# Optimization experiments

Hardware: AMD Instinct MI355X
Metric: run time of the kernel (lower is better)

Reference implementation:

```python
import jax, jax.numpy as jnp
import numpy as np

B, T, D_IN, N, O = 64, 512, 256, 1024, 128


def setup_inputs() -> dict:
    key = jax.random.key(0)
    k1, k2, k3, k4, k5 = jax.random.split(key, 5)
    X = jax.random.normal(k1, (B, T, D_IN), dtype=jnp.float32)
    # scale recurrent/input weights so tanh does not fully saturate
    Win = jax.random.normal(k2, (D_IN, N), dtype=jnp.float32) / np.sqrt(D_IN)
    W = jax.random.normal(k3, (N, N), dtype=jnp.float32) / np.sqrt(N)
    Wout = jax.random.normal(k4, (N, O), dtype=jnp.float32) / np.sqrt(N)
    bout = jax.random.normal(k5, (O,), dtype=jnp.float32)
    return {"X": X, "Win": Win, "W": W, "Wout": Wout, "bout": bout}


def reference(X, Win, W, Wout, bout):
    # Faithful to Model.evaluate:
    #   s[:, 0] = 0
    #   out = s @ Wout + bout
    b, t, _ = X.shape
    n = W.shape[0]
    s0 = jnp.zeros((b, n), dtype=X.dtype)

    def step(s, x):  # s: [B,N], x: [B,D_in]
        s_new = jnp.tanh(s @ W + x @ Win)
        return s_new, s_new

    xs = jnp.swapaxes(X[:, : t - 1, :], 0, 1)  # [T-1, B, D_in]
    _, s_seq = jax.lax.scan(step, s0, xs)  # [T-1, B, N]
    s = jnp.concatenate([s0[None], s_seq], axis=0)  # [T, B, N]
    s = jnp.swapaxes(s, 0, 1)  # [B, T, N]
    out = s @ Wout + bout  # [B, T, O]
    return (s, out)
```

## Files before the change

kernel.cpp:

```cpp
#include <hip/hip_runtime.h>

#define B_ 64
#define T_ 512
#define DIN_ 256
#define N_ 1024
#define O_ 128

using half8 = __attribute__((ext_vector_type(8))) _Float16;
using f32x4 = __attribute__((ext_vector_type(4))) float;
typedef unsigned long long ull;

__device__ __forceinline__ half8 cvt8(float4 a, float4 b) {
    half8 h;
    h[0] = (_Float16)a.x; h[1] = (_Float16)a.y; h[2] = (_Float16)a.z; h[3] = (_Float16)a.w;
    h[4] = (_Float16)b.x; h[5] = (_Float16)b.y; h[6] = (_Float16)b.z; h[7] = (_Float16)b.w;
    return h;
}

__device__ __forceinline__ float fast_tanh(float x) {
    float ax = __builtin_fabsf(x);
    float e  = __expf(-2.0f * ax);
    float r  = __fdividef(1.0f - e, 1.0f + e);
    return x < 0.0f ? -r : r;
}

__global__ void init_kernel(unsigned int* flags) {
    if (threadIdx.x < 128) flags[threadIdx.x] = 0u;
}

__global__ __launch_bounds__(512, 1) void rnn_kernel(
    const float* __restrict__ X,
    const float* __restrict__ W,
    const float* __restrict__ Win,
    float* __restrict__ s_out,
    _Float16* __restrict__ exch,
    unsigned int* __restrict__ flags)
{
    const int bs   = blockIdx.x & 3;
    const int cg   = blockIdx.x >> 2;
    const int tid  = threadIdx.x;
    const int wave = tid >> 6;
    const int lane = tid & 63;
    const int l15  = lane & 15;
    const int quad = lane >> 4;
    const int col0 = cg * 128 + wave * 16;
    const int arow = bs * 16 + l15;
    const int crow = bs * 16 + quad * 4;

    __shared__ _Float16 slab[16 * 1032];

    half8 wf[32];
    for (int p = 0; p < 8; ++p) {
        const int c = tid & 15, k0 = tid >> 4;
        const int wc = cg * 128 + p * 16 + c;
        for (int k = k0; k < N_; k += 32)
            slab[c * 1032 + k] = (_Float16)W[(size_t)k * N_ + wc];
        __syncthreads();
        if (wave == p) {
            #pragma unroll
            for (int kb = 0; kb < 32; ++kb)
                wf[kb] = *(const half8*)&slab[l15 * 1032 + kb * 32 + quad * 8];
        }
        __syncthreads();
    }
    half8 winf[8];
    for (int p = 0; p < 8; ++p) {
        const int c = tid & 15, k0 = tid >> 4;
        const int wc = cg * 128 + p * 16 + c;
        for (int k = k0; k < DIN_; k += 32)
            slab[c * 1032 + k] = (_Float16)Win[(size_t)k * N_ + wc];
        __syncthreads();
        if (wave == p) {
            #pragma unroll
            for (int kb = 0; kb < 8; ++kb)
                winf[kb] = *(const half8*)&slab[l15 * 1032 + kb * 32 + quad * 8];
        }
        __syncthreads();
    }

    #pragma unroll
    for (int i = 0; i < 4; ++i) {
        int e = i * 512 + tid;
        int r = e >> 7, c = e & 127;
        s_out[(size_t)(bs * 16 + r) * T_ * N_ + cg * 128 + c] = 0.0f;
    }

    f32x4 u = {0.f, 0.f, 0.f, 0.f};
    {
        const float* xp = X + (size_t)arow * T_ * DIN_ + quad * 8;
        #pragma unroll
        for (int kb = 0; kb < 8; ++kb) {
            float4 x0 = *(const float4*)(xp + kb * 32);
            float4 x1 = *(const float4*)(xp + kb * 32 + 4);
            u = __builtin_amdgcn_mfma_f32_16x16x32_f16(cvt8(x0, x1), winf[kb], u, 0, 0, 0);
        }
    }

    const int col   = col0 + l15;
    const int ebase = (col >> 5) * 512 + ((col >> 3) & 3) * 128 + quad * 32 + (col & 7);

    unsigned int* fl = flags + bs * 32;

    for (int t = 1; t < T_; ++t) {
        f32x4 acc0 = u;
        f32x4 acc1 = {0.f, 0.f, 0.f, 0.f};
        f32x4 acc2 = {0.f, 0.f, 0.f, 0.f};
        f32x4 acc3 = {0.f, 0.f, 0.f, 0.f};

        if (t >= 2) {
            const unsigned int tgt = (unsigned int)(t - 1);
            for (;;) {
                unsigned int v = tgt;
                if (lane < 8)
                    v = __hip_atomic_load(&fl[lane], __ATOMIC_RELAXED, __HIP_MEMORY_SCOPE_AGENT);
                if (__all((int)(v >= tgt))) break;
            }

            const ull* ep = (const ull*)(exch + (size_t)(bs * 2 + ((t - 1) & 1)) * 16384);
            ull r0 = __hip_atomic_load(&ep[tid],        __ATOMIC_RELAXED, __HIP_MEMORY_SCOPE_AGENT);
            ull r1 = __hip_atomic_load(&ep[tid + 512],  __ATOMIC_RELAXED, __HIP_MEMORY_SCOPE_AGENT);
            ull r2 = __hip_atomic_load(&ep[tid + 1024], __ATOMIC_RELAXED, __HIP_MEMORY_SCOPE_AGENT);
            ull r3 = __hip_atomic_load(&ep[tid + 1536], __ATOMIC_RELAXED, __HIP_MEMORY_SCOPE_AGENT);
            ull r4 = __hip_atomic_load(&ep[tid + 2048], __ATOMIC_RELAXED, __HIP_MEMORY_SCOPE_AGENT);
            ull r5 = __hip_atomic_load(&ep[tid + 2560], __ATOMIC_RELAXED, __HIP_MEMORY_SCOPE_AGENT);
            ull r6 = __hip_atomic_load(&ep[tid + 3072], __ATOMIC_RELAXED, __HIP_MEMORY_SCOPE_AGENT);
            ull r7 = __hip_atomic_load(&ep[tid + 3584], __ATOMIC_RELAXED, __HIP_MEMORY_SCOPE_AGENT);
            ull* lp = (ull*)slab;
            lp[tid]        = r0;
            lp[tid + 512]  = r1;
            lp[tid + 1024] = r2;
            lp[tid + 1536] = r3;
            lp[tid + 2048] = r4;
            lp[tid + 2560] = r5;
            lp[tid + 3072] = r6;
            lp[tid + 3584] = r7;
            __syncthreads();

            #pragma unroll
            for (int kb = 0; kb < 32; ++kb) {
                half8 a = *(const half8*)&slab[kb * 512 + lane * 8];
                if ((kb & 3) == 0)      acc0 = __builtin_amdgcn_mfma_f32_16x16x32_f16(a, wf[kb], acc0, 0, 0, 0);
                else if ((kb & 3) == 1) acc1 = __builtin_amdgcn_mfma_f32_16x16x32_f16(a, wf[kb], acc1, 0, 0, 0);
                else if ((kb & 3) == 2) acc2 = __builtin_amdgcn_mfma_f32_16x16x32_f16(a, wf[kb], acc2, 0, 0, 0);
                else                    acc3 = __builtin_amdgcn_mfma_f32_16x16x32_f16(a, wf[kb], acc3, 0, 0, 0);
            }
        }

        float v4[4];
        #pragma unroll
        for (int r = 0; r < 4; ++r)
            v4[r] = fast_tanh(acc0[r] + acc1[r] + acc2[r] + acc3[r]);

        _Float16* eb = exch + (size_t)(bs * 2 + (t & 1)) * 16384;
        #pragma unroll
        for (int r = 0; r < 4; ++r) {
            union { _Float16 h; unsigned short s; } cv;
            cv.h = (_Float16)v4[r];
            __hip_atomic_store((unsigned short*)(eb + ebase + r * 8), cv.s,
                               __ATOMIC_RELAXED, __HIP_MEMORY_SCOPE_AGENT);
        }
        __syncthreads();
        if (tid == 0)
            __hip_atomic_store(&fl[cg], (unsigned int)t,
                               __ATOMIC_RELAXED, __HIP_MEMORY_SCOPE_AGENT);

        #pragma unroll
        for (int r = 0; r < 4; ++r)
            s_out[(size_t)(crow + r) * T_ * N_ + (size_t)t * N_ + col] = v4[r];

        f32x4 un = {0.f, 0.f, 0.f, 0.f};
        if (t < T_ - 1) {
            const float* xp = X + ((size_t)arow * T_ + t) * DIN_ + quad * 8;
            #pragma unroll
            for (int kb = 0; kb < 8; ++kb) {
                float4 x0 = *(const float4*)(xp + kb * 32);
                float4 x1 = *(const float4*)(xp + kb * 32 + 4);
                un = __builtin_amdgcn_mfma_f32_16x16x32_f16(cvt8(x0, x1), winf[kb], un, 0, 0, 0);
            }
        }
        u = un;
    }
}

__global__ __launch_bounds__(256, 2) void out_gemm(
    const float* __restrict__ s_in,
    const float* __restrict__ Wout,
    const float* __restrict__ bout,
    float* __restrict__ outp)
{
    const int m0   = blockIdx.x * 128;
    const int tid  = threadIdx.x;
    const int wave = tid >> 6;
    const int lane = tid & 63;
    const int l15  = lane & 15;
    const int quad = lane >> 4;

    __shared__ _Float16 WoT[128][40];

    f32x4 acc[2][8];
    #pragma unroll
    for (int mf = 0; mf < 2; ++mf)
        #pragma unroll
        for (int nt = 0; nt < 8; ++nt) acc[mf][nt] = f32x4{0.f, 0.f, 0.f, 0.f};
    float bv[8];
    #pragma unroll
    for (int nt = 0; nt < 8; ++nt) bv[nt] = bout[nt * 16 + l15];

    for (int kb = 0; kb < 32; ++kb) {
        __syncthreads();
        #pragma unroll
        for (int i = 0; i < 16; ++i) {
            int e = i * 256 + tid;
            int c = e & 127, kk = e >> 7;
            WoT[c][kk] = (_Float16)Wout[(size_t)(kb * 32 + kk) * O_ + c];
        }
        __syncthreads();

        #pragma unroll
        for (int mf = 0; mf < 2; ++mf) {
            const float* ap = s_in + (size_t)(m0 + wave * 32 + mf * 16 + l15) * N_ + kb * 32 + quad * 8;
            float4 a0 = *(const float4*)ap;
            float4 a1 = *(const float4*)(ap + 4);
            half8 a = cvt8(a0, a1);
            #pragma unroll
            for (int nt = 0; nt < 8; ++nt) {
                half8 b = *(const half8*)&WoT[nt * 16 + l15][quad * 8];
                acc[mf][nt] = __builtin_amdgcn_mfma_f32_16x16x32_f16(a, b, acc[mf][nt], 0, 0, 0);
            }
        }
    }

    #pragma unroll
    for (int mf = 0; mf < 2; ++mf) {
        float* op = outp + (size_t)(m0 + wave * 32 + mf * 16 + quad * 4) * O_ + l15;
        #pragma unroll
        for (int nt = 0; nt < 8; ++nt)
            #pragma unroll
            for (int r = 0; r < 4; ++r)
                op[(size_t)r * O_ + nt * 16] = acc[mf][nt][r] + bv[nt];
    }
}

extern "C" void kernel_launch(void* const* d_in, const int* in_sizes, int n_in,
                              void* d_out, int out_size, void* d_ws, size_t ws_size,
                              hipStream_t stream) {
    const float* X    = (const float*)d_in[0];
    const float* Win  = (const float*)d_in[1];
    const float* W    = (const float*)d_in[2];
    const float* Wout = (const float*)d_in[3];
    const float* bout = (const float*)d_in[4];

    float* s_out = (float*)d_out;
    float* outp  = s_out + (size_t)B_ * T_ * N_;

    unsigned int* flags = (unsigned int*)d_ws;
    _Float16* exch = (_Float16*)((char*)d_ws + 1024);

    init_kernel<<<1, 128, 0, stream>>>(flags);
    rnn_kernel<<<32, 512, 0, stream>>>(X, W, Win, s_out, exch, flags);
    out_gemm<<<256, 256, 0, stream>>>(s_out, Wout, bout, outp);
}
```

Baseline: 3.223 ms.

## Replace per-block flags with step tags embedded in each exchange word

Removes the separate flag array and the post-store barrier plus flag publish. Each 64-bit exchange word now carries two packed fp16 state values and the timestep tag in its upper half, so consumers spin directly on the data until every tag matches. The load of the next step's data is issued speculatively right after the store to overlap latency. This doubles the exchange traffic per value and makes correctness depend on 64-bit atomic word visibility and the tag/parity scheme.

```diff
diff --git a/kernel.cpp b/kernel.cpp
--- a/kernel.cpp
+++ b/kernel.cpp
@@ -24,8 +24,14 @@
     return x < 0.0f ? -r : r;
 }
 
-__global__ void init_kernel(unsigned int* flags) {
-    if (threadIdx.x < 128) flags[threadIdx.x] = 0u;
+__device__ __forceinline__ unsigned pack2h(float a, float b) {
+    union { _Float16 h; unsigned short s; } ha, hb;
+    ha.h = (_Float16)a; hb.h = (_Float16)b;
+    return (unsigned)ha.s | ((unsigned)hb.s << 16);
+}
+
+__global__ void init_kernel(ull* exch) {
+    exch[(ull)blockIdx.x * blockDim.x + threadIdx.x] = 0ull;
 }
 
 __global__ __launch_bounds__(512, 1) void rnn_kernel(
@@ -33,8 +39,7 @@
     const float* __restrict__ W,
     const float* __restrict__ Win,
     float* __restrict__ s_out,
-    _Float16* __restrict__ exch,
-    unsigned int* __restrict__ flags)
+    ull* __restrict__ exch)
 {
     const int bs   = blockIdx.x & 3;
     const int cg   = blockIdx.x >> 2;
@@ -97,9 +102,14 @@
     }
 
     const int col   = col0 + l15;
-    const int ebase = (col >> 5) * 512 + ((col >> 3) & 3) * 128 + quad * 32 + (col & 7);
-
-    unsigned int* fl = flags + bs * 32;
+    const int colE  = col & ~1;
+    const int pidx0 = ((colE >> 5) * 512 + ((colE >> 3) & 3) * 128
+                       + quad * 32 + (colE & 7)) >> 1;
+    const bool odd  = (l15 & 1) != 0;
+    const int rbase = odd ? 2 : 0;
+
+    ull v[16];
+    const ull* rp = exch;
 
     for (int t = 1; t < T_; ++t) {
         f32x4 acc0 = u;
@@ -108,33 +118,23 @@
         f32x4 acc3 = {0.f, 0.f, 0.f, 0.f};
 
         if (t >= 2) {
-            const unsigned int tgt = (unsigned int)(t - 1);
+            const unsigned want = (unsigned)(t - 1);
             for (;;) {
-                unsigned int v = tgt;
-                if (lane < 8)
-                    v = __hip_atomic_load(&fl[lane], __ATOMIC_RELAXED, __HIP_MEMORY_SCOPE_AGENT);
-                if (__all((int)(v >= tgt))) break;
-            }
-
-            const ull* ep = (const ull*)(exch + (size_t)(bs * 2 + ((t - 1) & 1)) * 16384);
-            ull r0 = __hip_atomic_load(&ep[tid],        __ATOMIC_RELAXED, __HIP_MEMORY_SCOPE_AGENT);
-            ull r1 = __hip_atomic_load(&ep[tid + 512],  __ATOMIC_RELAXED, __HIP_MEMORY_SCOPE_AGENT);
-            ull r2 = __hip_atomic_load(&ep[tid + 1024], __ATOMIC_RELAXED, __HIP_MEMORY_SCOPE_AGENT);
-            ull r3 = __hip_atomic_load(&ep[tid + 1536], __ATOMIC_RELAXED, __HIP_MEMORY_SCOPE_AGENT);
-            ull r4 = __hip_atomic_load(&ep[tid + 2048], __ATOMIC_RELAXED, __HIP_MEMORY_SCOPE_AGENT);
-            ull r5 = __hip_atomic_load(&ep[tid + 2560], __ATOMIC_RELAXED, __HIP_MEMORY_SCOPE_AGENT);
-            ull r6 = __hip_atomic_load(&ep[tid + 3072], __ATOMIC_RELAXED, __HIP_MEMORY_SCOPE_AGENT);
-            ull r7 = __hip_atomic_load(&ep[tid + 3584], __ATOMIC_RELAXED, __HIP_MEMORY_SCOPE_AGENT);
-            ull* lp = (ull*)slab;
-            lp[tid]        = r0;
-            lp[tid + 512]  = r1;
-            lp[tid + 1024] = r2;
-            lp[tid + 1536] = r3;
-            lp[tid + 2048] = r4;
-            lp[tid + 2560] = r5;
-            lp[tid + 3072] = r6;
-            lp[tid + 3584] = r7;
-            __syncthreads();
+                bool ok = true;
+                #pragma unroll
+                for (int k = 0; k < 16; ++k)
+                    ok &= ((unsigned)(v[k] >> 32) == want);
+                if (ok) break;
+                #pragma unroll
+                for (int k = 0; k < 16; ++k)
+                    v[k] = __hip_atomic_load(&rp[tid + 512 * k],
+                                             __ATOMIC_RELAXED, __HIP_MEMORY_SCOPE_AGENT);
+            }
+            unsigned int* lp = (unsigned int*)slab;
+            #pragma unroll
+            for (int k = 0; k < 16; ++k)
+                lp[tid + 512 * k] = (unsigned int)v[k];
+            asm volatile("s_waitcnt lgkmcnt(0)\n\ts_barrier" ::: "memory");
 
             #pragma unroll
             for (int kb = 0; kb < 32; ++kb) {
@@ -151,18 +151,32 @@
         for (int r = 0; r < 4; ++r)
             v4[r] = fast_tanh(acc0[r] + acc1[r] + acc2[r] + acc3[r]);
 
-        _Float16* eb = exch + (size_t)(bs * 2 + (t & 1)) * 16384;
-        #pragma unroll
-        for (int r = 0; r < 4; ++r) {
-            union { _Float16 h; unsigned short s; } cv;
-            cv.h = (_Float16)v4[r];
-            __hip_atomic_store((unsigned short*)(eb + ebase + r * 8), cv.s,
+        ull* eb = exch + (size_t)(bs * 2 + (t & 1)) * 8192;
+        {
+            float q0 = __shfl_xor(v4[0], 1);
+            float q1 = __shfl_xor(v4[1], 1);
+            float q2 = __shfl_xor(v4[2], 1);
+            float q3 = __shfl_xor(v4[3], 1);
+            float e0 = odd ? q2 : v4[0];
+            float o0 = odd ? v4[2] : q0;
+            float e1 = odd ? q3 : v4[1];
+            float o1 = odd ? v4[3] : q1;
+            const ull tagbits = (ull)(unsigned)t << 32;
+            __hip_atomic_store(&eb[pidx0 + rbase * 4],
+                               (ull)pack2h(e0, o0) | tagbits,
                                __ATOMIC_RELAXED, __HIP_MEMORY_SCOPE_AGENT);
-        }
-        __syncthreads();
-        if (tid == 0)
-            __hip_atomic_store(&fl[cg], (unsigned int)t,
+            __hip_atomic_store(&eb[pidx0 + rbase * 4 + 4],
+                               (ull)pack2h(e1, o1) | tagbits,
                                __ATOMIC_RELAXED, __HIP_MEMORY_SCOPE_AGENT);
+        }
+
+        if (t < T_ - 1) {
+            rp = eb;
+            #pragma unroll
+            for (int k = 0; k < 16; ++k)
+                v[k] = __hip_atomic_load(&rp[tid + 512 * k],
+                                         __ATOMIC_RELAXED, __HIP_MEMORY_SCOPE_AGENT);
+        }
 
         #pragma unroll
         for (int r = 0; r < 4; ++r)
@@ -253,10 +267,9 @@
     float* s_out = (float*)d_out;
     float* outp  = s_out + (size_t)B_ * T_ * N_;
 
-    unsigned int* flags = (unsigned int*)d_ws;
-    _Float16* exch = (_Float16*)((char*)d_ws + 1024);
-
-    init_kernel<<<1, 128, 0, stream>>>(flags);
-    rnn_kernel<<<32, 512, 0, stream>>>(X, W, Win, s_out, exch, flags);
+    ull* exch = (ull*)d_ws;
+
+    init_kernel<<<64, 1024, 0, stream>>>(exch);
+    rnn_kernel<<<32, 512, 0, stream>>>(X, W, Win, s_out, exch);
     out_gemm<<<256, 256, 0, stream>>>(s_out, Wout, bout, outp);
 }
```

After: 4.919 ms. 1.53x slower.

## Replace per-block flag with per-wave sentinels and raw barriers in RNN step sync

Applied to the files above, without the earlier changes.

Each wave now publishes its own step counter after waiting only on its own global stores, so the block-wide __syncthreads before flag publication is gone. Consumers poll 64 per-wave sentinels (one per lane) instead of 8 per-block flags. The __syncthreads around the LDS slab fill is replaced with raw s_barrier plus an explicit lgkmcnt wait, with an extra barrier added so the slab is not overwritten while other waves still read it. This shortens the critical-path sync on each of the 511 serial steps, at the cost of more polling traffic and relying on hand-written waitcnt and barrier correctness.

```diff
diff --git a/kernel.cpp b/kernel.cpp
--- a/kernel.cpp
+++ b/kernel.cpp
@@ -24,8 +24,8 @@
     return x < 0.0f ? -r : r;
 }
 
-__global__ void init_kernel(unsigned int* flags) {
-    if (threadIdx.x < 128) flags[threadIdx.x] = 0u;
+__global__ void init_kernel(unsigned int* sent) {
+    sent[threadIdx.x] = 0u;
 }
 
 __global__ __launch_bounds__(512, 1) void rnn_kernel(
@@ -34,7 +34,7 @@
     const float* __restrict__ Win,
     float* __restrict__ s_out,
     _Float16* __restrict__ exch,
-    unsigned int* __restrict__ flags)
+    unsigned int* __restrict__ sent)
 {
     const int bs   = blockIdx.x & 3;
     const int cg   = blockIdx.x >> 2;
@@ -99,7 +99,8 @@
     const int col   = col0 + l15;
     const int ebase = (col >> 5) * 512 + ((col >> 3) & 3) * 128 + quad * 32 + (col & 7);
 
-    unsigned int* fl = flags + bs * 32;
+    unsigned int* sp = sent + bs * 64;
+    const int mysent = cg * 8 + wave;
 
     for (int t = 1; t < T_; ++t) {
         f32x4 acc0 = u;
@@ -108,12 +109,11 @@
         f32x4 acc3 = {0.f, 0.f, 0.f, 0.f};
 
         if (t >= 2) {
-            const unsigned int tgt = (unsigned int)(t - 1);
+            const unsigned want = (unsigned)(t - 1);
             for (;;) {
-                unsigned int v = tgt;
-                if (lane < 8)
-                    v = __hip_atomic_load(&fl[lane], __ATOMIC_RELAXED, __HIP_MEMORY_SCOPE_AGENT);
-                if (__all((int)(v >= tgt))) break;
+                unsigned v = __hip_atomic_load(&sp[lane], __ATOMIC_RELAXED,
+                                               __HIP_MEMORY_SCOPE_AGENT);
+                if (__all((int)(v >= want))) break;
             }
 
             const ull* ep = (const ull*)(exch + (size_t)(bs * 2 + ((t - 1) & 1)) * 16384);
@@ -125,6 +125,9 @@
             ull r5 = __hip_atomic_load(&ep[tid + 2560], __ATOMIC_RELAXED, __HIP_MEMORY_SCOPE_AGENT);
             ull r6 = __hip_atomic_load(&ep[tid + 3072], __ATOMIC_RELAXED, __HIP_MEMORY_SCOPE_AGENT);
             ull r7 = __hip_atomic_load(&ep[tid + 3584], __ATOMIC_RELAXED, __HIP_MEMORY_SCOPE_AGENT);
+
+            asm volatile("s_barrier" ::: "memory");
+
             ull* lp = (ull*)slab;
             lp[tid]        = r0;
             lp[tid + 512]  = r1;
@@ -134,7 +137,7 @@
             lp[tid + 2560] = r5;
             lp[tid + 3072] = r6;
             lp[tid + 3584] = r7;
-            __syncthreads();
+            asm volatile("s_waitcnt lgkmcnt(0)\n\ts_barrier" ::: "memory");
 
             #pragma unroll
             for (int kb = 0; kb < 32; ++kb) {
@@ -159,9 +162,9 @@
             __hip_atomic_store((unsigned short*)(eb + ebase + r * 8), cv.s,
                                __ATOMIC_RELAXED, __HIP_MEMORY_SCOPE_AGENT);
         }
-        __syncthreads();
-        if (tid == 0)
-            __hip_atomic_store(&fl[cg], (unsigned int)t,
+        asm volatile("s_waitcnt vmcnt(0)" ::: "memory");
+        if (lane == 0)
+            __hip_atomic_store(&sp[mysent], (unsigned int)t,
                                __ATOMIC_RELAXED, __HIP_MEMORY_SCOPE_AGENT);
 
         #pragma unroll
@@ -253,10 +256,10 @@
     float* s_out = (float*)d_out;
     float* outp  = s_out + (size_t)B_ * T_ * N_;
 
-    unsigned int* flags = (unsigned int*)d_ws;
-    _Float16* exch = (_Float16*)((char*)d_ws + 1024);
-
-    init_kernel<<<1, 128, 0, stream>>>(flags);
-    rnn_kernel<<<32, 512, 0, stream>>>(X, W, Win, s_out, exch, flags);
+    unsigned int* sent = (unsigned int*)d_ws;
+    _Float16* exch = (_Float16*)((char*)d_ws + 4096);
+
+    init_kernel<<<1, 256, 0, stream>>>(sent);
+    rnn_kernel<<<32, 512, 0, stream>>>(X, W, Win, s_out, exch, sent);
     out_gemm<<<256, 256, 0, stream>>>(s_out, Wout, bout, outp);
 }
```

After: 3.219 ms. No clear change (-0.1%).
